# Optimization experiments

Measured on AMD Instinct MI355X. Metric: run time of the kernel, lower is better.

The kernel has to match this reference:

```python
import jax, jax.numpy as jnp
import numpy as np

N_FEATURES = 1024
N_HEADS = 16
D_ATTN = 64


def setup_inputs() -> dict:
    key = jax.random.key(0)
    k_x, k_qkv, k_pw, k_pb = jax.random.split(key, 4)
    B, S = 2, 2048
    x = jax.random.normal(k_x, (B, S, N_FEATURES), dtype=jnp.float32)
    # torch nn.Linear weights are [out, in]; init scale ~ 1/sqrt(in)
    w_qkv = jax.random.normal(k_qkv, (3 * N_HEADS * D_ATTN, N_FEATURES), dtype=jnp.float32) / np.sqrt(N_FEATURES)
    w_proj = jax.random.normal(k_pw, (N_FEATURES, N_HEADS * D_ATTN), dtype=jnp.float32) / np.sqrt(N_HEADS * D_ATTN)
    b_proj = jax.random.normal(k_pb, (N_FEATURES,), dtype=jnp.float32) / np.sqrt(N_HEADS * D_ATTN)
    return {"x": x, "w_qkv": w_qkv, "w_proj": w_proj, "b_proj": b_proj}


def reference(x, w_qkv, w_proj, b_proj):
    B, S, F = x.shape
    H, D = N_HEADS, D_ATTN
    # fused QKV projection (bias=False): [B,S,3*H*D]
    qkv = jnp.einsum('bsf,of->bso', x, w_qkv)
    qkv = qkv.reshape(B, S, 3, H, D)
    q = jnp.transpose(qkv[:, :, 0], (0, 2, 1, 3))  # [B,H,S,D]
    k = jnp.transpose(qkv[:, :, 1], (0, 2, 1, 3))
    v = jnp.transpose(qkv[:, :, 2], (0, 2, 1, 3))
    scale = 1.0 / jnp.sqrt(jnp.asarray(D, dtype=x.dtype))
    scores = jnp.einsum('bhqd,bhkd->bhqk', q, k) * scale  # [B,H,S,S]
    attn = jax.nn.softmax(scores, axis=-1)
    out = jnp.einsum('bhqk,bhkd->bhqd', attn, v)  # [B,H,S,D]
    out = jnp.transpose(out, (0, 2, 1, 3)).reshape(B, S, H * D)
    # output projection (dropout is identity in eval mode)
    return jnp.einsum('bsm,fm->bsf', out, w_proj) + b_proj
```

## Files before the change

### kernel.cpp

```cpp
#include <hip/hip_runtime.h>
#include <hip/hip_bf16.h>
#include <math.h>

#define BATCH 2
#define SEQ 2048
#define NFEAT 1024
#define NHEAD 16
#define DHEAD 64
#define MROWS (BATCH * SEQ)
#define NQKV (3 * NHEAD * DHEAD)

typedef __attribute__((ext_vector_type(8))) short short8;
typedef __attribute__((ext_vector_type(4))) float floatx4;
typedef __attribute__((ext_vector_type(16))) float floatx16;
typedef __attribute__((ext_vector_type(4))) unsigned int uintx4;

#define CEXP 0.18033688f

__device__ __forceinline__ unsigned short f2bf(float f) {
    unsigned int u = __float_as_uint(f);
    u += 0x7fff + ((u >> 16) & 1);
    return (unsigned short)(u >> 16);
}

__device__ __forceinline__ float fast_exp2(float x) {
    return __builtin_amdgcn_exp2f(x);
}

__device__ __forceinline__ uint pack_bf16x2(float lo, float hi) {
    float2 t; t.x = lo; t.y = hi;
    __hip_bfloat162 h = __float22bfloat162_rn(t);
    union { __hip_bfloat162 h; uint u; } c; c.h = h;
    return c.u;
}

__device__ __forceinline__ void async16(const void* g, void* l) {
    __builtin_amdgcn_global_load_lds(
        (const __attribute__((address_space(1))) void*)g,
        (__attribute__((address_space(3))) void*)l, 16, 0, 0);
}

__global__ void cvt_swz(const float* __restrict__ x, const float* __restrict__ wq,
                        const float* __restrict__ wp,
                        ushort* __restrict__ xb, ushort* __restrict__ wqb,
                        ushort* __restrict__ wpb) {
    const int NX = MROWS * NFEAT / 4, NWQ = NQKV * NFEAT / 4, NWP = NFEAT * NFEAT / 4;
    int i = blockIdx.x * blockDim.x + threadIdx.x;
    if (i >= NX + NWQ + NWP) return;
    const float* src; ushort* dst; int idx4;
    if (i < NX)            { src = x;  dst = xb;  idx4 = i; }
    else if (i < NX + NWQ) { src = wq; dst = wqb; idx4 = i - NX; }
    else                   { src = wp; dst = wpb; idx4 = i - NX - NWQ; }
    float4 v = ((const float4*)src)[idx4];
    ushort4 o;
    o.x = f2bf(v.x); o.y = f2bf(v.y); o.z = f2bf(v.z); o.w = f2bf(v.w);
    const int e = idx4 * 4;
    const int k = e & (NFEAT - 1);
    const int row = e >> 10;
    const int kp = (k & ~31) | (((((k >> 3) & 3) ^ ((row >> 1) & 3))) << 3) | (k & 7);
    *(ushort4*)(dst + (size_t)row * NFEAT + kp) = o;
}

__global__ __launch_bounds__(256, 3)
void gemm_qkv(const ushort* __restrict__ A, const ushort* __restrict__ W,
              ushort* __restrict__ qb, ushort* __restrict__ kb, ushort* __restrict__ vtb) {
    __shared__ ushort smem[16384];
    ushort* As = smem;
    ushort* Bs = smem + 8192;
    const int tid = threadIdx.x;
    const int wave = tid >> 6, lane = tid & 63;
    const int id = blockIdx.x;
    const int xcd = id & 7, slot = id >> 3;
    const int by = (xcd >> 1) * 8 + slot / 12;
    const int bx = (xcd & 1) * 12 + slot % 12;
    const int m0 = by * 128, n0 = bx * 128;
    const int wm = (wave >> 1) * 64, wn = (wave & 1) * 64;
    const int lr = lane & 15, lg = lane >> 4;
    const int kswz = (lg ^ ((lr >> 1) & 3)) * 8;

    floatx4 acc[4][4] = {};

    for (int k0 = 0; k0 < NFEAT; k0 += 64) {
#pragma unroll
        for (int q = 0; q < 4; ++q) {
            const int s = q * 256 + tid;
            const int row = s >> 3, kc = (s & 7) * 8;
            async16(A + (size_t)(m0 + row) * NFEAT + k0 + kc, (void*)(As + s * 8));
            async16(W + (size_t)(n0 + row) * NFEAT + k0 + kc, (void*)(Bs + s * 8));
        }
        __syncthreads();
#pragma unroll
        for (int kk = 0; kk < 2; ++kk) {
            short8 a[4], b[4];
#pragma unroll
            for (int i = 0; i < 4; ++i)
                a[i] = *(const short8*)(As + (wm + i * 16 + lr) * 64 + kk * 32 + kswz);
#pragma unroll
            for (int j = 0; j < 4; ++j)
                b[j] = *(const short8*)(Bs + (wn + j * 16 + lr) * 64 + kk * 32 + kswz);
#pragma unroll
            for (int i = 0; i < 4; ++i)
#pragma unroll
                for (int j = 0; j < 4; ++j)
                    acc[i][j] = __builtin_amdgcn_mfma_f32_16x16x32_bf16(a[i], b[j], acc[i][j], 0, 0, 0);
        }
        __syncthreads();
    }

    const int t = n0 >> 10;
    const int bidx = m0 >> 11;
    if (t < 2) {
#pragma unroll
        for (int i = 0; i < 4; ++i)
#pragma unroll
            for (int j = 0; j < 4; ++j)
#pragma unroll
                for (int r = 0; r < 4; ++r) {
                    const int m = m0 + wm + i * 16 + lg * 4 + r;
                    const int n = n0 + wn + j * 16 + lr;
                    const int s = m & (SEQ - 1);
                    const int rem = n & 1023, h = rem >> 6, d = rem & 63;
                    if (t == 0) {
                        qb[((size_t)(bidx * NHEAD + h) * SEQ + s) * DHEAD + d] =
                            f2bf(acc[i][j][r] * CEXP);
                    } else {
                        const int dcol = ((((d >> 3) ^ (s & 7)) << 3)) | (d & 7);
                        kb[((size_t)(bidx * NHEAD + h) * SEQ + s) * DHEAD + dcol] =
                            f2bf(acc[i][j][r]);
                    }
                }
    } else {
#pragma unroll
        for (int hhalf = 0; hhalf < 2; ++hhalf) {
            if ((wm >> 6) == hhalf) {
#pragma unroll
                for (int i = 0; i < 4; ++i) {
                    const int chunk = i * 2 + (lg >> 1);
#pragma unroll
                    for (int j = 0; j < 4; ++j) {
                        const int n = wn + j * 16 + lr;
                        uint2 pk;
                        pk.x = pack_bf16x2(acc[i][j][0], acc[i][j][1]);
                        pk.y = pack_bf16x2(acc[i][j][2], acc[i][j][3]);
                        *(uint2*)(smem + n * 64 + ((chunk ^ (n & 7)) * 8) + (lg & 1) * 4) = pk;
                    }
                }
            }
            __syncthreads();
            const int s_base = (m0 & (SEQ - 1)) + hhalf * 64;
#pragma unroll
            for (int it = 0; it < 4; ++it) {
                const int n_r = (tid >> 3) + it * 32;
                const int p = tid & 7;
                short8 rowv = *(const short8*)(smem + n_r * 64 + p * 8);
                const int nglob = n0 + n_r;
                const int d = nglob & 63, hh = (nglob & 1023) >> 6;
                *(short8*)(vtb + ((size_t)(bidx * NHEAD + hh) * DHEAD + d) * SEQ + s_base + p * 8) = rowv;
            }
            __syncthreads();
        }
    }
}

__global__ __launch_bounds__(256, 2)
void gemm_proj(const ushort* __restrict__ A, const ushort* __restrict__ W,
               const float* __restrict__ bias, float* __restrict__ Cout) {
    __shared__ ushort As[128 * 64];
    __shared__ ushort Bs[64 * 64];
    const int tid = threadIdx.x;
    const int wave = tid >> 6, lane = tid & 63;
    const int id = blockIdx.x;
    const int xcd = id & 7, slot = id >> 3;
    const int by = (xcd >> 1) * 8 + (slot >> 3);
    const int bx = (xcd & 1) * 8 + (slot & 7);
    const int m0 = by * 128, n0 = bx * 64;
    const int wm = (wave >> 1) * 64, wn = (wave & 1) * 32;
    const int lr = lane & 15, lg = lane >> 4;
    const int kswz = (lg ^ ((lr >> 1) & 3)) * 8;

    floatx4 acc[4][2] = {};

    for (int k0 = 0; k0 < NFEAT; k0 += 64) {
#pragma unroll
        for (int q = 0; q < 4; ++q) {
            const int s = q * 256 + tid;
            const int row = s >> 3, kc = (s & 7) * 8;
            async16(A + (size_t)(m0 + row) * NFEAT + k0 + kc, (void*)(As + s * 8));
        }
#pragma unroll
        for (int q = 0; q < 2; ++q) {
            const int s = q * 256 + tid;
            const int row = s >> 3, kc = (s & 7) * 8;
            async16(W + (size_t)(n0 + row) * NFEAT + k0 + kc, (void*)(Bs + s * 8));
        }
        __syncthreads();
#pragma unroll
        for (int kk = 0; kk < 2; ++kk) {
            short8 a[4], b[2];
#pragma unroll
            for (int i = 0; i < 4; ++i)
                a[i] = *(const short8*)(As + (wm + i * 16 + lr) * 64 + kk * 32 + kswz);
#pragma unroll
            for (int j = 0; j < 2; ++j)
                b[j] = *(const short8*)(Bs + (wn + j * 16 + lr) * 64 + kk * 32 + kswz);
#pragma unroll
            for (int i = 0; i < 4; ++i)
#pragma unroll
                for (int j = 0; j < 2; ++j)
                    acc[i][j] = __builtin_amdgcn_mfma_f32_16x16x32_bf16(a[i], b[j], acc[i][j], 0, 0, 0);
        }
        __syncthreads();
    }

#pragma unroll
    for (int i = 0; i < 4; ++i)
#pragma unroll
        for (int j = 0; j < 2; ++j)
#pragma unroll
            for (int r = 0; r < 4; ++r) {
                const int m = m0 + wm + i * 16 + lg * 4 + r;
                const int n = n0 + wn + j * 16 + lr;
                Cout[(size_t)m * NFEAT + n] = acc[i][j][r] + bias[n];
            }
}

__global__ __launch_bounds__(256, 2)
void flash_attn(const ushort* __restrict__ qb, const ushort* __restrict__ kb,
                const ushort* __restrict__ vtb, ushort* __restrict__ aob) {
    const int id = blockIdx.x;
    const int xcd = id & 7, slot = id >> 3;
    const int bh = xcd + 8 * (slot >> 4);
    const int qt = slot & 15;
    const int tid = threadIdx.x, wave = tid >> 6, lane = tid & 63;
    const int l31 = lane & 31, l5 = lane >> 5;
    const int swz = lane & 7;

    __shared__ ushort Ks[2][64 * 64];
    __shared__ ushort Vs[2][64 * 64];

    const ushort* Qb = qb + (size_t)bh * SEQ * DHEAD;
    const ushort* Kb = kb + (size_t)bh * SEQ * DHEAD;
    const ushort* Vt = vtb + (size_t)bh * DHEAD * SEQ;

    const int q0 = qt * 128 + wave * 32;

    short8 qf[4];
#pragma unroll
    for (int kw = 0; kw < 4; ++kw)
        qf[kw] = *(const short8*)(Qb + (size_t)(q0 + l31) * DHEAD + kw * 16 + l5 * 8);

    const int kofs = tid * 8;
    const size_t vrow = (size_t)(tid >> 3) * SEQ;
    const int vcol = (tid & 7) * 8;

    async16(Kb + kofs,                    (void*)(Ks[0] + kofs));
    async16(Kb + 2048 + kofs,             (void*)(Ks[0] + 2048 + kofs));
    async16(Vt + vrow + vcol,             (void*)(Vs[0] + kofs));
    async16(Vt + 32 * SEQ + vrow + vcol,  (void*)(Vs[0] + 2048 + kofs));

    floatx16 acc_o[2] = {};
    float l_lane = 0.0f;

#define FLASH_PREFETCH(BUF, KV)                                                     \
    {                                                                               \
        const int kv_ = (KV);                                                       \
        async16(Kb + (size_t)kv_ * DHEAD + kofs,          (void*)(Ks[BUF] + kofs)); \
        async16(Kb + (size_t)kv_ * DHEAD + 2048 + kofs,   (void*)(Ks[BUF] + 2048 + kofs)); \
        async16(Vt + vrow + kv_ + vcol,                   (void*)(Vs[BUF] + kofs)); \
        async16(Vt + 32 * SEQ + vrow + kv_ + vcol,        (void*)(Vs[BUF] + 2048 + kofs)); \
    }

#define FLASH_COMPUTE(BUF)                                                          \
    {                                                                               \
        floatx16 st[2] = {};                                                        \
        __builtin_amdgcn_s_setprio(1);                                              \
        _Pragma("unroll")                                                           \
        for (int kw = 0; kw < 4; ++kw) {                                            \
            _Pragma("unroll")                                                       \
            for (int i = 0; i < 2; ++i) {                                           \
                short8 kf = *(const short8*)(Ks[BUF] + (i * 32 + l31) * 64 +        \
                                             (((kw * 2 + l5) ^ swz) * 8));          \
                st[i] = __builtin_amdgcn_mfma_f32_32x32x16_bf16(kf, qf[kw], st[i], 0, 0, 0); \
            }                                                                       \
        }                                                                           \
        __builtin_amdgcn_s_setprio(0);                                              \
        uintx4 pa[4];                                                               \
        _Pragma("unroll")                                                           \
        for (int i = 0; i < 2; ++i) {                                               \
            uint P2[8];                                                             \
            _Pragma("unroll")                                                       \
            for (int rr = 0; rr < 8; ++rr) {                                        \
                const float p0 = fast_exp2(st[i][rr * 2]);                          \
                const float p1 = fast_exp2(st[i][rr * 2 + 1]);                      \
                l_lane += p0 + p1;                                                  \
                P2[rr] = pack_bf16x2(p0, p1);                                       \
            }                                                                       \
            _Pragma("unroll")                                                       \
            for (int r3 = 0; r3 < 2; ++r3) {                                        \
                _Pragma("unroll")                                                   \
                for (int r1 = 0; r1 < 2; ++r1) {                                    \
                    uint a = P2[r3 * 4 + r1];                            \
                    uint b = P2[r3 * 4 + 2 + r1];                        \
                    asm volatile("v_permlane32_swap_b32 %0, %1" : "+v"(a), "+v"(b)); \
                    pa[i * 2 + r3][r1] = a;               \
                    pa[i * 2 + r3][2 + r1] = b;           \
                }                                                                   \
            }                                                                       \
        }                                                                           \
        __builtin_amdgcn_s_setprio(1);                                              \
        _Pragma("unroll")                                                           \
        for (int kk = 0; kk < 4; ++kk) {                                            \
            const short8 paf = *(const short8*)&pa[kk];                             \
            _Pragma("unroll")                                                       \
            for (int j2 = 0; j2 < 2; ++j2) {                                        \
                short8 vf = *(const short8*)(Vs[BUF] + (j2 * 32 + l31) * 64 +       \
                                             (((kk * 2 + l5) ^ swz) * 8));          \
                acc_o[j2] = __builtin_amdgcn_mfma_f32_32x32x16_bf16(paf, vf, acc_o[j2], 0, 0, 0); \
            }                                                                       \
        }                                                                           \
        __builtin_amdgcn_s_setprio(0);                                              \
    }

    for (int kt = 0; kt < SEQ / 64; kt += 2) {
        __syncthreads();
        FLASH_PREFETCH(1, (kt + 1) * 64)
        FLASH_COMPUTE(0)
        __syncthreads();
        if (kt + 2 < SEQ / 64)
            FLASH_PREFETCH(0, (kt + 2) * 64)
        FLASH_COMPUTE(1)
    }
#undef FLASH_PREFETCH
#undef FLASH_COMPUTE

    l_lane += __shfl_xor(l_lane, 32);
    const float invl = 1.0f / l_lane;

    const int b = bh >> 4, h = bh & 15;
#pragma unroll
    for (int r = 0; r < 16; ++r) {
        const int qrow = (r & 3) + 4 * l5 + 8 * (r >> 2);
        const float il = __shfl(invl, qrow);
        const int srow = b * SEQ + q0 + qrow;
        const int key = (srow >> 1) & 3;
#pragma unroll
        for (int j2 = 0; j2 < 2; ++j2) {
            const int d = j2 * 32 + l31;
            const int dsw = (d & ~31) | ((((d >> 3) & 3) ^ key) << 3) | (d & 7);
            aob[(size_t)srow * (NHEAD * DHEAD) + h * DHEAD + dsw] = f2bf(acc_o[j2][r] * il);
        }
    }
}

extern "C" void kernel_launch(void* const* d_in, const int* in_sizes, int n_in,
                              void* d_out, int out_size, void* d_ws, size_t ws_size,
                              hipStream_t stream) {
    const float* x      = (const float*)d_in[0];
    const float* w_qkv  = (const float*)d_in[1];
    const float* w_proj = (const float*)d_in[2];
    const float* b_proj = (const float*)d_in[3];
    float* out = (float*)d_out;

    ushort* ws = (ushort*)d_ws;
    ushort* xb     = ws;
    ushort* wqkvb  = xb + (size_t)MROWS * NFEAT;
    ushort* wprojb = wqkvb + (size_t)NQKV * NFEAT;
    ushort* qb     = wprojb + (size_t)NFEAT * NFEAT;
    ushort* kb     = qb + (size_t)MROWS * NFEAT;
    ushort* vtb    = kb + (size_t)MROWS * NFEAT;
    ushort* aob    = vtb + (size_t)MROWS * NFEAT;

    {
        const int total = (MROWS * NFEAT + NQKV * NFEAT + NFEAT * NFEAT) / 4;
        cvt_swz<<<(total + 255) / 256, 256, 0, stream>>>(x, w_qkv, w_proj, xb, wqkvb, wprojb);
    }

    {
        gemm_qkv<<<768, 256, 0, stream>>>(xb, wqkvb, qb, kb, vtb);
    }

    {
        flash_attn<<<512, 256, 0, stream>>>(qb, kb, vtb, aob);
    }

    {
        gemm_proj<<<512, 256, 0, stream>>>(aob, wprojb, b_proj, out);
    }
}
```

Measured before the change: 176.1 us.

## Split KV sequence across two wave groups in flash attention and merge in LDS

Flash attention blocks grow from 256 to 512 threads. Each half of the waves processes one half of the KV sequence, using separate double-buffered K/V tiles, and the partial outputs and row sums are merged through shared memory before normalisation. The aim is to raise wave-level parallelism and latency hiding per Q tile by halving each wave's serial KV loop. The cost is doubled LDS, an extra reduction phase, and stricter register limits from launch bounds of 512 threads and 4 blocks per CU.

```diff
diff --git a/kernel.cpp b/kernel.cpp
--- a/kernel.cpp
+++ b/kernel.cpp
@@ -224,7 +224,7 @@
             }
 }
 
-__global__ __launch_bounds__(256, 2)
+__global__ __launch_bounds__(512, 4)
 void flash_attn(const ushort* __restrict__ qb, const ushort* __restrict__ kb,
                 const ushort* __restrict__ vtb, ushort* __restrict__ aob) {
     const int id = blockIdx.x;
@@ -234,15 +234,17 @@
     const int tid = threadIdx.x, wave = tid >> 6, lane = tid & 63;
     const int l31 = lane & 31, l5 = lane >> 5;
     const int swz = lane & 7;
-
-    __shared__ ushort Ks[2][64 * 64];
-    __shared__ ushort Vs[2][64 * 64];
+    const int kvh = wave >> 2;
+    const int qw = wave & 3;
+
+    __shared__ ushort Ks[2][2][64 * 64];
+    __shared__ ushort Vs[2][2][64 * 64];
 
     const ushort* Qb = qb + (size_t)bh * SEQ * DHEAD;
     const ushort* Kb = kb + (size_t)bh * SEQ * DHEAD;
     const ushort* Vt = vtb + (size_t)bh * DHEAD * SEQ;
 
-    const int q0 = qt * 128 + wave * 32;
+    const int q0 = qt * 128 + qw * 32;
 
     short8 qf[4];
 #pragma unroll
@@ -253,10 +255,8 @@
     const size_t vrow = (size_t)(tid >> 3) * SEQ;
     const int vcol = (tid & 7) * 8;
 
-    async16(Kb + kofs,                    (void*)(Ks[0] + kofs));
-    async16(Kb + 2048 + kofs,             (void*)(Ks[0] + 2048 + kofs));
-    async16(Vt + vrow + vcol,             (void*)(Vs[0] + kofs));
-    async16(Vt + 32 * SEQ + vrow + vcol,  (void*)(Vs[0] + 2048 + kofs));
+    const ushort* KsW = &Ks[kvh][0][0];
+    const ushort* VsW = &Vs[kvh][0][0];
 
     floatx16 acc_o[2] = {};
     float l_lane = 0.0f;
@@ -264,10 +264,10 @@
 #define FLASH_PREFETCH(BUF, KV)                                                     \
     {                                                                               \
         const int kv_ = (KV);                                                       \
-        async16(Kb + (size_t)kv_ * DHEAD + kofs,          (void*)(Ks[BUF] + kofs)); \
-        async16(Kb + (size_t)kv_ * DHEAD + 2048 + kofs,   (void*)(Ks[BUF] + 2048 + kofs)); \
-        async16(Vt + vrow + kv_ + vcol,                   (void*)(Vs[BUF] + kofs)); \
-        async16(Vt + 32 * SEQ + vrow + kv_ + vcol,        (void*)(Vs[BUF] + 2048 + kofs)); \
+        async16(Kb + (size_t)kv_ * DHEAD + kofs,            (void*)(Ks[0][BUF] + kofs)); \
+        async16(Kb + (size_t)(1024 + kv_) * DHEAD + kofs,   (void*)(Ks[1][BUF] + kofs)); \
+        async16(Vt + vrow + kv_ + vcol,                     (void*)(Vs[0][BUF] + kofs)); \
+        async16(Vt + vrow + 1024 + kv_ + vcol,              (void*)(Vs[1][BUF] + kofs)); \
     }
 
 #define FLASH_COMPUTE(BUF)                                                          \
@@ -278,7 +278,7 @@
         for (int kw = 0; kw < 4; ++kw) {                                            \
             _Pragma("unroll")                                                       \
             for (int i = 0; i < 2; ++i) {                                           \
-                short8 kf = *(const short8*)(Ks[BUF] + (i * 32 + l31) * 64 +        \
+                short8 kf = *(const short8*)(KsW + (BUF) * 4096 + (i * 32 + l31) * 64 + \
                                              (((kw * 2 + l5) ^ swz) * 8));          \
                 st[i] = __builtin_amdgcn_mfma_f32_32x32x16_bf16(kf, qf[kw], st[i], 0, 0, 0); \
             }                                                                       \
@@ -313,7 +313,7 @@
             const short8 paf = *(const short8*)&pa[kk];                             \
             _Pragma("unroll")                                                       \
             for (int j2 = 0; j2 < 2; ++j2) {                                        \
-                short8 vf = *(const short8*)(Vs[BUF] + (j2 * 32 + l31) * 64 +       \
+                short8 vf = *(const short8*)(VsW + (BUF) * 4096 + (j2 * 32 + l31) * 64 + \
                                              (((kk * 2 + l5) ^ swz) * 8));          \
                 acc_o[j2] = __builtin_amdgcn_mfma_f32_32x32x16_bf16(paf, vf, acc_o[j2], 0, 0, 0); \
             }                                                                       \
@@ -321,33 +321,67 @@
         __builtin_amdgcn_s_setprio(0);                                              \
     }
 
-    for (int kt = 0; kt < SEQ / 64; kt += 2) {
-        __syncthreads();
-        FLASH_PREFETCH(1, (kt + 1) * 64)
+    FLASH_PREFETCH(0, 0)
+
+    for (int kt = 0; kt < 1024; kt += 128) {
+        __syncthreads();
+        FLASH_PREFETCH(1, kt + 64)
         FLASH_COMPUTE(0)
         __syncthreads();
-        if (kt + 2 < SEQ / 64)
-            FLASH_PREFETCH(0, (kt + 2) * 64)
+        if (kt + 128 < 1024)
+            FLASH_PREFETCH(0, kt + 128)
         FLASH_COMPUTE(1)
     }
 #undef FLASH_PREFETCH
 #undef FLASH_COMPUTE
 
-    l_lane += __shfl_xor(l_lane, 32);
-    const float invl = 1.0f / l_lane;
-
-    const int b = bh >> 4, h = bh & 15;
-#pragma unroll
-    for (int r = 0; r < 16; ++r) {
-        const int qrow = (r & 3) + 4 * l5 + 8 * (r >> 2);
-        const float il = __shfl(invl, qrow);
-        const int srow = b * SEQ + q0 + qrow;
-        const int key = (srow >> 1) & 3;
-#pragma unroll
-        for (int j2 = 0; j2 < 2; ++j2) {
-            const int d = j2 * 32 + l31;
-            const int dsw = (d & ~31) | ((((d >> 3) & 3) ^ key) << 3) | (d & 7);
-            aob[(size_t)srow * (NHEAD * DHEAD) + h * DHEAD + dsw] = f2bf(acc_o[j2][r] * il);
+    __syncthreads();
+    float* mrg = (float*)&Ks[0][0][0];
+    if (wave >= 4) {
+        float* p = mrg + (size_t)(wave - 4) * 2304 + lane * 36;
+#pragma unroll
+        for (int j2 = 0; j2 < 2; ++j2)
+#pragma unroll
+            for (int r4 = 0; r4 < 4; ++r4) {
+                floatx4 v;
+                v[0] = acc_o[j2][r4 * 4 + 0];
+                v[1] = acc_o[j2][r4 * 4 + 1];
+                v[2] = acc_o[j2][r4 * 4 + 2];
+                v[3] = acc_o[j2][r4 * 4 + 3];
+                *(floatx4*)(p + j2 * 16 + r4 * 4) = v;
+            }
+        p[32] = l_lane;
+    }
+    __syncthreads();
+    if (wave < 4) {
+        const float* p = mrg + (size_t)wave * 2304 + lane * 36;
+#pragma unroll
+        for (int j2 = 0; j2 < 2; ++j2)
+#pragma unroll
+            for (int r4 = 0; r4 < 4; ++r4) {
+                floatx4 v = *(const floatx4*)(p + j2 * 16 + r4 * 4);
+#pragma unroll
+                for (int e = 0; e < 4; ++e)
+                    acc_o[j2][r4 * 4 + e] += v[e];
+            }
+        l_lane += p[32];
+
+        l_lane += __shfl_xor(l_lane, 32);
+        const float invl = 1.0f / l_lane;
+
+        const int b = bh >> 4, h = bh & 15;
+#pragma unroll
+        for (int r = 0; r < 16; ++r) {
+            const int qrow = (r & 3) + 4 * l5 + 8 * (r >> 2);
+            const float il = __shfl(invl, qrow);
+            const int srow = b * SEQ + q0 + qrow;
+            const int key = (srow >> 1) & 3;
+#pragma unroll
+            for (int j2 = 0; j2 < 2; ++j2) {
+                const int d = j2 * 32 + l31;
+                const int dsw = (d & ~31) | ((((d >> 3) & 3) ^ key) << 3) | (d & 7);
+                aob[(size_t)srow * (NHEAD * DHEAD) + h * DHEAD + dsw] = f2bf(acc_o[j2][r] * il);
+            }
         }
     }
 }
@@ -380,7 +414,7 @@
     }
 
     {
-        flash_attn<<<512, 256, 0, stream>>>(qb, kb, vtb, aob);
+        flash_attn<<<512, 512, 0, stream>>>(qb, kb, vtb, aob);
     }
 
     {
```

Result: no change. 176.2 us (median of 2 runs) (+0.0%).
